# Kernel tuning notes

Hardware: AMD Instinct MI355X
Metric: run time of the kernel (lower is better)

Reference implementation:

```python
import jax, jax.numpy as jnp
import numpy as np

D_MODEL = 2048
N_HEADS = 16
D_HEAD = 128
ROPE_BASE = 10000.0


def setup_inputs() -> dict:
    key = jax.random.key(0)
    ks = jax.random.split(key, 5)
    s = 0.02
    x = jax.random.normal(ks[0], (2, 4096, D_MODEL), dtype=jnp.float32)
    Wq = jax.random.normal(ks[1], (N_HEADS * D_HEAD, D_MODEL), dtype=jnp.float32) * s
    Wk = jax.random.normal(ks[2], (N_HEADS * D_HEAD, D_MODEL), dtype=jnp.float32) * s
    Wv = jax.random.normal(ks[3], (N_HEADS * D_HEAD, D_MODEL), dtype=jnp.float32) * s
    Wo = jax.random.normal(ks[4], (D_MODEL, N_HEADS * D_HEAD), dtype=jnp.float32) * s
    return {"x": x, "Wq": Wq, "Wk": Wk, "Wv": Wv, "Wo": Wo}


def _rope_tables(seq_len, dtype):
    inv_freq = 1.0 / (ROPE_BASE ** (jnp.arange(0, D_HEAD, 2, dtype=jnp.float32) / D_HEAD))
    freqs = jnp.arange(seq_len, dtype=jnp.float32)[:, None] * inv_freq[None, :]  # (S, D/2)
    cos = jnp.repeat(jnp.cos(freqs), 2, axis=-1).astype(dtype)  # (S, D)
    sin = jnp.repeat(jnp.sin(freqs), 2, axis=-1).astype(dtype)
    return cos, sin


def _rotate_half(x):
    # interleaved pairs: (x0,x1,...) -> (-x1,x0,-x3,x2,...)
    x1 = x[..., ::2]
    x2 = x[..., 1::2]
    return jnp.stack([-x2, x1], axis=-1).reshape(x.shape)


def reference(x, Wq, Wk, Wv, Wo):
    B, S, _ = x.shape
    H, D = N_HEADS, D_HEAD
    q = jnp.einsum('bsd,ed->bse', x, Wq).reshape(B, S, H, D).transpose(0, 2, 1, 3)
    k = jnp.einsum('bsd,ed->bse', x, Wk).reshape(B, S, H, D).transpose(0, 2, 1, 3)
    v = jnp.einsum('bsd,ed->bse', x, Wv).reshape(B, S, H, D).transpose(0, 2, 1, 3)
    cos, sin = _rope_tables(S, x.dtype)  # (S, D)
    q = q * cos + _rotate_half(q) * sin
    k = k * cos + _rotate_half(k) * sin
    # causal scaled dot-product attention
    scale = 1.0 / jnp.sqrt(jnp.asarray(D, dtype=x.dtype))
    scores = jnp.einsum('bhqd,bhkd->bhqk', q, k) * scale
    mask = jnp.tril(jnp.ones((S, S), dtype=bool))
    scores = jnp.where(mask, scores, jnp.finfo(x.dtype).min)
    probs = jax.nn.softmax(scores, axis=-1)
    a = jnp.einsum('bhqk,bhkd->bhqd', probs, v)
    a = a.transpose(0, 2, 1, 3).reshape(B, S, H * D)
    return jnp.einsum('bse,de->bsd', a, Wo)
```

## Files before the change

### kernel.cpp

```cpp
#include <hip/hip_runtime.h>

typedef float f32x4 __attribute__((ext_vector_type(4)));
typedef float f32x16 __attribute__((ext_vector_type(16)));
typedef short bf16x8 __attribute__((ext_vector_type(8)));

#define DEVI __device__ __forceinline__

constexpr int Bn = 2;
constexpr int Sn = 4096;
constexpr int Hn = 16;
constexpr int Dn = 128;
constexpr int En = 2048;
constexpr int Mtot = Bn * Sn;

DEVI unsigned short f2bf(float f) {
  unsigned u = __float_as_uint(f);
  u += 0x7fffu + ((u >> 16) & 1u);
  return (unsigned short)(u >> 16);
}
DEVI float bf2f(unsigned short h) {
  return __uint_as_float(((unsigned)h) << 16);
}
DEVI unsigned pk2(float a, float b) {
  return (unsigned)f2bf(a) | ((unsigned)f2bf(b) << 16);
}

DEVI void async16(const void* g, void* l) {
  __builtin_amdgcn_global_load_lds(
      (const __attribute__((address_space(1))) void*)g,
      (__attribute__((address_space(3))) void*)l, 16, 0, 0);
}

DEVI bf16x8 pack_pa(float a0, float a1, float a2, float a3,
                    float a4, float a5, float a6, float a7, int hi) {
  unsigned w0 = pk2(a0, a1), w1 = pk2(a2, a3);
  unsigned y0 = pk2(a4, a5), y1 = pk2(a6, a7);
  unsigned x0 = __shfl_xor(w0, 32), x1 = __shfl_xor(w1, 32);
  unsigned z0 = __shfl_xor(y0, 32), z1 = __shfl_xor(y1, 32);
  union { unsigned u[4]; bf16x8 v; } r;
  r.u[0] = hi ? z0 : w0;
  r.u[1] = hi ? z1 : w1;
  r.u[2] = hi ? y0 : x0;
  r.u[3] = hi ? y1 : x1;
  return r.v;
}

__global__ void cvt_kernel(const float* __restrict__ in, ushort* __restrict__ out) {
  size_t i = ((size_t)blockIdx.x * 256 + threadIdx.x) * 4;
  float4 v = *(const float4*)&in[i];
  ushort4 o;
  o.x = f2bf(v.x); o.y = f2bf(v.y); o.z = f2bf(v.z); o.w = f2bf(v.w);
  *(ushort4*)&out[i] = o;
}

__global__ void rope_kernel(ushort* __restrict__ Q, float scale) {
  int row = blockIdx.x;
  int s = row & (Sn - 1);
  int t = threadIdx.x;
  size_t base = (size_t)row * En;
#pragma unroll
  for (int rep = 0; rep < 4; ++rep) {
    int p = rep * 256 + t;
    int e = p * 2;
    int pp = (e & (Dn - 1)) >> 1;
    float inv = exp2f(-(float)pp * (13.287712379549449f / 64.0f));
    float ang = (float)s * inv;
    float c = cosf(ang), sn = sinf(ang);
    unsigned v = *(unsigned*)&Q[base + e];
    float q0 = bf2f((unsigned short)(v & 0xffffu));
    float q1 = bf2f((unsigned short)(v >> 16));
    float n0 = (q0 * c - q1 * sn) * scale;
    float n1 = (q1 * c + q0 * sn) * scale;
    unsigned outv = (unsigned)f2bf(n0) | ((unsigned)f2bf(n1) << 16);
    *(unsigned*)&Q[base + e] = outv;
  }
}

template <int EPI>
__global__ __launch_bounds__(256) void gemm_bt(const ushort* __restrict__ A,
                                               const ushort* __restrict__ Bm,
                                               void* __restrict__ Cv) {
  __shared__ ushort As[128 * 64];
  __shared__ ushort Bs[128 * 64];
  const int t = threadIdx.x;
  const int lane = t & 63, w = t >> 6;
  const int ln = lane & 15, gq = lane >> 4;
  const int m0 = blockIdx.y * 128, n0 = blockIdx.x * 128;
  const int rm = (w >> 1) * 64, rn = (w & 1) * 64;
  f32x4 acc[4][4] = {};

  for (int k0 = 0; k0 < En; k0 += 64) {
#pragma unroll
    for (int rep = 0; rep < 4; ++rep) {
      int c = rep * 256 + t;
      int row = c >> 3, c8 = c & 7;
      async16(&A[(size_t)(m0 + row) * En + k0 + c8 * 8],
              (char*)As + (rep * 256 + w * 64) * 16);
      async16(&Bm[(size_t)(n0 + row) * En + k0 + c8 * 8],
              (char*)Bs + (rep * 256 + w * 64) * 16);
    }
    __syncthreads();
#pragma unroll
    for (int kk = 0; kk < 64; kk += 32) {
      bf16x8 af[4], bf[4];
#pragma unroll
      for (int i = 0; i < 4; ++i)
        af[i] = *(const bf16x8*)&As[(rm + i * 16 + ln) * 64 + kk + gq * 8];
#pragma unroll
      for (int j = 0; j < 4; ++j)
        bf[j] = *(const bf16x8*)&Bs[(rn + j * 16 + ln) * 64 + kk + gq * 8];
#pragma unroll
      for (int i = 0; i < 4; ++i)
#pragma unroll
        for (int j = 0; j < 4; ++j)
          acc[i][j] = __builtin_amdgcn_mfma_f32_16x16x32_bf16(af[i], bf[j], acc[i][j], 0, 0, 0);
    }
    __syncthreads();
  }

  if constexpr (EPI == 0) {
    ushort* C = (ushort*)Cv;
#pragma unroll
    for (int i = 0; i < 4; ++i) {
      int row0 = m0 + rm + i * 16 + gq * 4;
#pragma unroll
      for (int j = 0; j < 4; ++j) {
        int col = n0 + rn + j * 16 + ln;
#pragma unroll
        for (int r = 0; r < 4; ++r)
          C[(size_t)(row0 + r) * En + col] = f2bf(acc[i][j][r]);
      }
    }
  } else if constexpr (EPI == 1) {
    ushort* Vt = (ushort*)Cv;
#pragma unroll
    for (int i = 0; i < 4; ++i) {
      int mrow = m0 + rm + i * 16 + gq * 4;
      int bb = mrow >> 12;
      int ss = mrow & (Sn - 1);
#pragma unroll
      for (int j = 0; j < 4; ++j) {
        int col = n0 + rn + j * 16 + ln;
        ushort4 pk;
        pk.x = f2bf(acc[i][j][0]); pk.y = f2bf(acc[i][j][1]);
        pk.z = f2bf(acc[i][j][2]); pk.w = f2bf(acc[i][j][3]);
        *(ushort4*)&Vt[((size_t)(bb * En + col)) * Sn + ss] = pk;
      }
    }
  } else {
    float* C = (float*)Cv;
#pragma unroll
    for (int i = 0; i < 4; ++i) {
      int row0 = m0 + rm + i * 16 + gq * 4;
#pragma unroll
      for (int j = 0; j < 4; ++j) {
        int col = n0 + rn + j * 16 + ln;
#pragma unroll
        for (int r = 0; r < 4; ++r)
          C[(size_t)(row0 + r) * En + col] = acc[i][j][r];
      }
    }
  }
}

__global__ __launch_bounds__(256) void flash_kernel(const ushort* __restrict__ Qb,
                                                    const ushort* __restrict__ Kb,
                                                    const ushort* __restrict__ Vt,
                                                    ushort* __restrict__ Ab) {
  __shared__ ushort Ks[64 * 128];
  __shared__ ushort Vs[128 * 64];
  const int t = threadIdx.x;
  const int lane = t & 63, w = t >> 6;
  const int l31 = lane & 31, hi = lane >> 5;

  const int orig = blockIdx.x;
  const int pos = orig >> 3;
  const int bh = ((orig & 7) << 2) + (pos >> 5);
  const int qt = 31 - (pos & 31);
  const int q0 = qt * 128;
  const int b = bh >> 4, h = bh & 15;

  const int qrow = q0 + w * 32 + l31;

  bf16x8 qf[8];
  {
    size_t qbase = ((size_t)(b * Sn + qrow)) * En + h * Dn + hi * 8;
#pragma unroll
    for (int ks = 0; ks < 8; ++ks)
      qf[ks] = *(const bf16x8*)&Qb[qbase + ks * 16];
  }

  f32x16 o[4] = {};
  float m_prev = -1e30f, l_prev = 0.f;
  const int last = 2 * qt + 1;

  for (int tt = 0; tt <= last; ++tt) {
    const int j0 = tt << 6;
#pragma unroll
    for (int rep = 0; rep < 4; ++rep) {
      int c = rep * 256 + t;
      int krow = c >> 4, ksl = c & 15;
      int kc = ksl ^ (krow & 15);
      async16(&Kb[((size_t)(b * Sn + j0 + krow)) * En + h * Dn + kc * 8],
              (char*)Ks + (rep * 256 + w * 64) * 16);
      int vrow = c >> 3, vsl = c & 7;
      int vc = vsl ^ (vrow & 7);
      async16(&Vt[((size_t)(b * En + h * Dn + vrow)) * Sn + j0 + vc * 8],
              (char*)Vs + (rep * 256 + w * 64) * 16);
    }
    __syncthreads();

    if (j0 <= q0 + w * 32 + 31) {
      f32x16 s0 = {}, s1 = {};
      __builtin_amdgcn_s_setprio(1);
#pragma unroll
      for (int ks = 0; ks < 8; ++ks) {
        int soff = ((ks * 2 + hi) ^ (l31 & 15)) << 3;
        bf16x8 kf0 = *(const bf16x8*)&Ks[l31 * 128 + soff];
        bf16x8 kf1 = *(const bf16x8*)&Ks[(32 + l31) * 128 + soff];
        s0 = __builtin_amdgcn_mfma_f32_32x32x16_bf16(kf0, qf[ks], s0, 0, 0, 0);
        s1 = __builtin_amdgcn_mfma_f32_32x32x16_bf16(kf1, qf[ks], s1, 0, 0, 0);
      }
      __builtin_amdgcn_s_setprio(0);

      float mx = -1e30f;
      if (j0 + 63 > q0 + w * 32) {
#pragma unroll
        for (int r = 0; r < 16; ++r) {
          int jj = j0 + (r & 3) + 8 * (r >> 2) + 4 * hi;
          if (jj > qrow) s0[r] = -1e30f;
          if (jj + 32 > qrow) s1[r] = -1e30f;
          mx = fmaxf(mx, fmaxf(s0[r], s1[r]));
        }
      } else {
#pragma unroll
        for (int r = 0; r < 16; ++r)
          mx = fmaxf(mx, fmaxf(s0[r], s1[r]));
      }
      mx = fmaxf(mx, __shfl_xor(mx, 32));

      float mn;
      if (__all(mx - m_prev <= 8.f)) {
        mn = m_prev;
      } else {
        mn = fmaxf(m_prev, mx);
        float alpha = exp2f(m_prev - mn);
        m_prev = mn;
        l_prev *= alpha;
#pragma unroll
        for (int d = 0; d < 4; ++d) o[d] *= alpha;
      }
      float sum = 0.f;
#pragma unroll
      for (int r = 0; r < 16; ++r) {
        float p0 = exp2f(s0[r] - mn);
        float p1 = exp2f(s1[r] - mn);
        s0[r] = p0; s1[r] = p1;
        sum += p0 + p1;
      }
      sum += __shfl_xor(sum, 32);
      l_prev += sum;

      bf16x8 pa[4];
      pa[0] = pack_pa(s0[0], s0[1], s0[2], s0[3], s0[4], s0[5], s0[6], s0[7], hi);
      pa[1] = pack_pa(s0[8], s0[9], s0[10], s0[11], s0[12], s0[13], s0[14], s0[15], hi);
      pa[2] = pack_pa(s1[0], s1[1], s1[2], s1[3], s1[4], s1[5], s1[6], s1[7], hi);
      pa[3] = pack_pa(s1[8], s1[9], s1[10], s1[11], s1[12], s1[13], s1[14], s1[15], hi);

      __builtin_amdgcn_s_setprio(1);
#pragma unroll
      for (int dsub = 0; dsub < 4; ++dsub) {
        int d = dsub * 32 + l31;
#pragma unroll
        for (int ks = 0; ks < 4; ++ks) {
          int soff = ((ks * 2 + hi) ^ (d & 7)) << 3;
          bf16x8 vf = *(const bf16x8*)&Vs[d * 64 + soff];
          o[dsub] = __builtin_amdgcn_mfma_f32_32x32x16_bf16(vf, pa[ks], o[dsub], 0, 0, 0);
        }
      }
      __builtin_amdgcn_s_setprio(0);
    }
    __syncthreads();
  }

  float inv = 1.f / l_prev;
  size_t base = ((size_t)(b * Sn + qrow)) * En + h * Dn;
#pragma unroll
  for (int dsub = 0; dsub < 4; ++dsub) {
#pragma unroll
    for (int g = 0; g < 4; ++g) {
      ushort4 pk;
      pk.x = f2bf(o[dsub][g * 4 + 0] * inv);
      pk.y = f2bf(o[dsub][g * 4 + 1] * inv);
      pk.z = f2bf(o[dsub][g * 4 + 2] * inv);
      pk.w = f2bf(o[dsub][g * 4 + 3] * inv);
      *(ushort4*)&Ab[base + dsub * 32 + g * 8 + hi * 4] = pk;
    }
  }
}

extern "C" void kernel_launch(void* const* d_in, const int* in_sizes, int n_in,
                              void* d_out, int out_size, void* d_ws, size_t ws_size,
                              hipStream_t stream) {
  const float* x  = (const float*)d_in[0];
  const float* Wq = (const float*)d_in[1];
  const float* Wk = (const float*)d_in[2];
  const float* Wv = (const float*)d_in[3];
  const float* Wo = (const float*)d_in[4];

  char* ws = (char*)d_ws;
  ushort* xb  = (ushort*)(ws + 0);
  ushort* wqb = (ushort*)(ws + 33554432);
  ushort* wkb = (ushort*)(ws + 41943040);
  ushort* wvb = (ushort*)(ws + 50331648);
  ushort* wob = (ushort*)(ws + 58720256);
  ushort* Qb  = (ushort*)(ws + 67108864);
  ushort* Kb  = (ushort*)(ws + 100663296);
  ushort* Vt  = (ushort*)(ws + 134217728);
  ushort* Ab  = xb;

  cvt_kernel<<<dim3(Mtot * En / 1024), 256, 0, stream>>>(x, xb);
  cvt_kernel<<<dim3(En * En / 1024), 256, 0, stream>>>(Wq, wqb);
  cvt_kernel<<<dim3(En * En / 1024), 256, 0, stream>>>(Wk, wkb);
  cvt_kernel<<<dim3(En * En / 1024), 256, 0, stream>>>(Wv, wvb);
  cvt_kernel<<<dim3(En * En / 1024), 256, 0, stream>>>(Wo, wob);

  dim3 ggrid(En / 128, Mtot / 128);
  gemm_bt<0><<<ggrid, 256, 0, stream>>>(xb, wqb, (void*)Qb);
  gemm_bt<0><<<ggrid, 256, 0, stream>>>(xb, wkb, (void*)Kb);
  gemm_bt<1><<<ggrid, 256, 0, stream>>>(xb, wvb, (void*)Vt);

  rope_kernel<<<dim3(Mtot), 256, 0, stream>>>(Qb, 0.08838834764831845f * 1.4426950408889634f);
  rope_kernel<<<dim3(Mtot), 256, 0, stream>>>(Kb, 1.0f);

  flash_kernel<<<dim3(Bn * Hn * Sn / 128), 256, 0, stream>>>(Qb, Kb, Vt, Ab);

  gemm_bt<2><<<ggrid, 256, 0, stream>>>(Ab, wob, d_out);
}
```

Measured before the change: 943.5 us.

## Fuse RoPE into QK projection epilogue and double-buffer flash attention K/V tiles

After: 2.184 ms. 2.31x slower.

```diff
diff --git a/kernel.cpp b/kernel.cpp
--- a/kernel.cpp
+++ b/kernel.cpp
@@ -53,33 +53,11 @@
   *(ushort4*)&out[i] = o;
 }
 
-__global__ void rope_kernel(ushort* __restrict__ Q, float scale) {
-  int row = blockIdx.x;
-  int s = row & (Sn - 1);
-  int t = threadIdx.x;
-  size_t base = (size_t)row * En;
-#pragma unroll
-  for (int rep = 0; rep < 4; ++rep) {
-    int p = rep * 256 + t;
-    int e = p * 2;
-    int pp = (e & (Dn - 1)) >> 1;
-    float inv = exp2f(-(float)pp * (13.287712379549449f / 64.0f));
-    float ang = (float)s * inv;
-    float c = cosf(ang), sn = sinf(ang);
-    unsigned v = *(unsigned*)&Q[base + e];
-    float q0 = bf2f((unsigned short)(v & 0xffffu));
-    float q1 = bf2f((unsigned short)(v >> 16));
-    float n0 = (q0 * c - q1 * sn) * scale;
-    float n1 = (q1 * c + q0 * sn) * scale;
-    unsigned outv = (unsigned)f2bf(n0) | ((unsigned)f2bf(n1) << 16);
-    *(unsigned*)&Q[base + e] = outv;
-  }
-}
-
 template <int EPI>
 __global__ __launch_bounds__(256) void gemm_bt(const ushort* __restrict__ A,
                                                const ushort* __restrict__ Bm,
-                                               void* __restrict__ Cv) {
+                                               void* __restrict__ Cv,
+                                               float scale) {
   __shared__ ushort As[128 * 64];
   __shared__ ushort Bs[128 * 64];
   const int t = threadIdx.x;
@@ -147,7 +125,7 @@
         *(ushort4*)&Vt[((size_t)(bb * En + col)) * Sn + ss] = pk;
       }
     }
-  } else {
+  } else if constexpr (EPI == 2) {
     float* C = (float*)Cv;
 #pragma unroll
     for (int i = 0; i < 4; ++i) {
@@ -160,15 +138,38 @@
           C[(size_t)(row0 + r) * En + col] = acc[i][j][r];
       }
     }
-  }
-}
-
-__global__ __launch_bounds__(256) void flash_kernel(const ushort* __restrict__ Qb,
-                                                    const ushort* __restrict__ Kb,
-                                                    const ushort* __restrict__ Vt,
-                                                    ushort* __restrict__ Ab) {
-  __shared__ ushort Ks[64 * 128];
-  __shared__ ushort Vs[128 * 64];
+  } else {
+    ushort* C = (ushort*)Cv;
+    const int odd = ln & 1;
+#pragma unroll
+    for (int i = 0; i < 4; ++i) {
+      int row0 = m0 + rm + i * 16 + gq * 4;
+#pragma unroll
+      for (int j = 0; j < 4; ++j) {
+        int col = n0 + rn + j * 16 + ln;
+        int pp = (col & (Dn - 1)) >> 1;
+        float inv = exp2f(-(float)pp * (13.287712379549449f / 64.0f));
+#pragma unroll
+        for (int r = 0; r < 4; ++r) {
+          int row = row0 + r;
+          float ang = (float)(row & (Sn - 1)) * inv;
+          float cs = cosf(ang), sn = sinf(ang);
+          float self = acc[i][j][r];
+          float other = __shfl_xor(self, 1);
+          float val = odd ? (self * cs + other * sn) : (self * cs - other * sn);
+          C[(size_t)row * En + col] = f2bf(val * scale);
+        }
+      }
+    }
+  }
+}
+
+__global__ __launch_bounds__(256, 2) void flash_kernel(const ushort* __restrict__ Qb,
+                                                       const ushort* __restrict__ Kb,
+                                                       const ushort* __restrict__ Vt,
+                                                       ushort* __restrict__ Ab) {
+  __shared__ ushort Ks[2][64 * 128];
+  __shared__ ushort Vs[2][128 * 64];
   const int t = threadIdx.x;
   const int lane = t & 63, w = t >> 6;
   const int l31 = lane & 31, hi = lane >> 5;
@@ -194,21 +195,35 @@
   float m_prev = -1e30f, l_prev = 0.f;
   const int last = 2 * qt + 1;
 
-  for (int tt = 0; tt <= last; ++tt) {
-    const int j0 = tt << 6;
+  auto stage = [&](int jt0, int bufi) {
 #pragma unroll
     for (int rep = 0; rep < 4; ++rep) {
       int c = rep * 256 + t;
       int krow = c >> 4, ksl = c & 15;
       int kc = ksl ^ (krow & 15);
-      async16(&Kb[((size_t)(b * Sn + j0 + krow)) * En + h * Dn + kc * 8],
-              (char*)Ks + (rep * 256 + w * 64) * 16);
+      async16(&Kb[((size_t)(b * Sn + jt0 + krow)) * En + h * Dn + kc * 8],
+              (char*)&Ks[bufi][0] + (rep * 256 + w * 64) * 16);
       int vrow = c >> 3, vsl = c & 7;
       int vc = vsl ^ (vrow & 7);
-      async16(&Vt[((size_t)(b * En + h * Dn + vrow)) * Sn + j0 + vc * 8],
-              (char*)Vs + (rep * 256 + w * 64) * 16);
-    }
-    __syncthreads();
+      async16(&Vt[((size_t)(b * En + h * Dn + vrow)) * Sn + jt0 + vc * 8],
+              (char*)&Vs[bufi][0] + (rep * 256 + w * 64) * 16);
+    }
+  };
+
+  stage(0, 0);
+
+  for (int tt = 0; tt <= last; ++tt) {
+    const int cur = tt & 1;
+    const int j0 = tt << 6;
+    __builtin_amdgcn_s_barrier();
+    if (tt < last) {
+      stage((tt + 1) << 6, cur ^ 1);
+      asm volatile("s_waitcnt vmcnt(8)" ::: "memory");
+    } else {
+      asm volatile("s_waitcnt vmcnt(0)" ::: "memory");
+    }
+    __builtin_amdgcn_s_barrier();
+    __builtin_amdgcn_sched_barrier(0);
 
     if (j0 <= q0 + w * 32 + 31) {
       f32x16 s0 = {}, s1 = {};
@@ -216,8 +231,8 @@
 #pragma unroll
       for (int ks = 0; ks < 8; ++ks) {
         int soff = ((ks * 2 + hi) ^ (l31 & 15)) << 3;
-        bf16x8 kf0 = *(const bf16x8*)&Ks[l31 * 128 + soff];
-        bf16x8 kf1 = *(const bf16x8*)&Ks[(32 + l31) * 128 + soff];
+        bf16x8 kf0 = *(const bf16x8*)&Ks[cur][l31 * 128 + soff];
+        bf16x8 kf1 = *(const bf16x8*)&Ks[cur][(32 + l31) * 128 + soff];
         s0 = __builtin_amdgcn_mfma_f32_32x32x16_bf16(kf0, qf[ks], s0, 0, 0, 0);
         s1 = __builtin_amdgcn_mfma_f32_32x32x16_bf16(kf1, qf[ks], s1, 0, 0, 0);
       }
@@ -274,13 +289,12 @@
 #pragma unroll
         for (int ks = 0; ks < 4; ++ks) {
           int soff = ((ks * 2 + hi) ^ (d & 7)) << 3;
-          bf16x8 vf = *(const bf16x8*)&Vs[d * 64 + soff];
+          bf16x8 vf = *(const bf16x8*)&Vs[cur][d * 64 + soff];
           o[dsub] = __builtin_amdgcn_mfma_f32_32x32x16_bf16(vf, pa[ks], o[dsub], 0, 0, 0);
         }
       }
       __builtin_amdgcn_s_setprio(0);
     }
-    __syncthreads();
   }
 
   float inv = 1.f / l_prev;
@@ -326,14 +340,12 @@
   cvt_kernel<<<dim3(En * En / 1024), 256, 0, stream>>>(Wo, wob);
 
   dim3 ggrid(En / 128, Mtot / 128);
-  gemm_bt<0><<<ggrid, 256, 0, stream>>>(xb, wqb, (void*)Qb);
-  gemm_bt<0><<<ggrid, 256, 0, stream>>>(xb, wkb, (void*)Kb);
-  gemm_bt<1><<<ggrid, 256, 0, stream>>>(xb, wvb, (void*)Vt);
-
-  rope_kernel<<<dim3(Mtot), 256, 0, stream>>>(Qb, 0.08838834764831845f * 1.4426950408889634f);
-  rope_kernel<<<dim3(Mtot), 256, 0, stream>>>(Kb, 1.0f);
+  gemm_bt<3><<<ggrid, 256, 0, stream>>>(xb, wqb, (void*)Qb,
+                                        0.08838834764831845f * 1.4426950408889634f);
+  gemm_bt<3><<<ggrid, 256, 0, stream>>>(xb, wkb, (void*)Kb, 1.0f);
+  gemm_bt<1><<<ggrid, 256, 0, stream>>>(xb, wvb, (void*)Vt, 0.f);
 
   flash_kernel<<<dim3(Bn * Hn * Sn / 128), 256, 0, stream>>>(Qb, Kb, Vt, Ab);
 
-  gemm_bt<2><<<ggrid, 256, 0, stream>>>(Ab, wob, d_out);
-}
+  gemm_bt<2><<<ggrid, 256, 0, stream>>>(Ab, wob, d_out, 0.f);
+}
```
